# Kernel tuning notes

Measured on AMD Instinct MI355X. Metric: run time of the kernel, lower is better.

The kernel has to match this reference:

```python
import jax, jax.numpy as jnp
import numpy as np

B = 131072
SD, AD, HID = 24, 8, 32
NH = SD + AD            # n_heads = 32
UNITS = HID * NH        # 1024


def _xavier(k, shape):
    fan_in, fan_out = shape[-2], shape[-1]
    lim = float(np.sqrt(6.0 / (fan_in + fan_out)))
    return jax.random.uniform(k, shape, jnp.float32, -lim, lim)


def setup_inputs() -> dict:
    key = jax.random.key(0)
    ks = jax.random.split(key, 8)
    return dict(
        state=jax.random.normal(ks[0], (B, SD), jnp.float32),
        action=jax.random.normal(ks[1], (B, AD), jnp.float32),
        # ripple layer 1: per-head Linear(NH -> HID), gate logits init 0 (init_prob=0.5)
        W1=_xavier(ks[2], (NH, NH, HID)), b1=jnp.zeros((NH, HID), jnp.float32), g1=jnp.zeros((NH,), jnp.float32),
        # ripple layer 2: per-head Linear(UNITS -> HID)
        W2=_xavier(ks[3], (NH, UNITS, HID)), b2=jnp.zeros((NH, HID), jnp.float32), g2=jnp.zeros((NH,), jnp.float32),
        # q_network
        Wq1=_xavier(ks[4], (UNITS, 256)), bq1=jnp.zeros((256,), jnp.float32),
        ln1_g=jnp.ones((256,), jnp.float32), ln1_b=jnp.zeros((256,), jnp.float32),
        Wq2=_xavier(ks[5], (256, 128)), bq2=jnp.zeros((128,), jnp.float32),
        ln2_g=jnp.ones((128,), jnp.float32), ln2_b=jnp.zeros((128,), jnp.float32),
        Wq3=_xavier(ks[6], (128, 1)), bq3=jnp.zeros((1,), jnp.float32),
    )


def _ripple(x, W, b, g):
    # x: [B, D]; W: [H, D, K]; per-head linear + tanh, scaled by per-head sigmoid gate
    h = jnp.tanh(jnp.einsum('bd,hdk->bhk', x, W) + b[None])  # [B, H, K]
    h = h * jax.nn.sigmoid(g)[None, :, None]
    return h.reshape(x.shape[0], -1)  # [B, H*K]


def _ln(x, g, b, eps=1e-5):
    mu = jnp.mean(x, -1, keepdims=True)
    var = jnp.mean((x - mu) ** 2, -1, keepdims=True)
    return (x - mu) * jax.lax.rsqrt(var + eps) * g + b


def reference(state, action, W1, b1, g1, W2, b2, g2,
              Wq1, bq1, ln1_g, ln1_b, Wq2, bq2, ln2_g, ln2_b, Wq3, bq3):
    sa = jnp.concatenate([state, action], axis=1)          # [B, SD+AD]
    x = _ripple(sa, W1, b1, g1)                            # [B, UNITS]
    x = _ripple(x, W2, b2, g2)                             # [B, UNITS]
    h = jax.nn.relu(_ln(x @ Wq1 + bq1, ln1_g, ln1_b))      # [B, 256] (dropout = eval identity)
    h = jax.nn.relu(_ln(h @ Wq2 + bq2, ln2_g, ln2_b))      # [B, 128]
    return h @ Wq3 + bq3                                   # [B, 1]
```

## Files before the change

### kernel.cpp

```cpp
#include <hip/hip_runtime.h>
#include <hip/hip_bf16.h>

typedef _Float16 f16x8 __attribute__((ext_vector_type(8)));
typedef _Float16 f16x4 __attribute__((ext_vector_type(4)));
typedef float f32x4 __attribute__((ext_vector_type(4)));

__device__ __forceinline__ float tanh_fast(float x) {
  float e = __expf(2.0f * x);
  return 1.0f - 2.0f * __builtin_amdgcn_rcpf(e + 1.0f);
}
__device__ __forceinline__ float sigmoid_fast(float x) {
  return __builtin_amdgcn_rcpf(1.0f + __expf(-x));
}

__global__ __launch_bounds__(256) void prep_weights(
    const float* __restrict__ W1, const float* __restrict__ W2,
    const float* __restrict__ Wq1, const float* __restrict__ Wq2,
    _Float16* __restrict__ V1p, _Float16* __restrict__ V2p,
    _Float16* __restrict__ T1p, _Float16* __restrict__ T2p) {
  __shared__ float S[32 * 33];
  int b = blockIdx.x, t = threadIdx.x;
  if (b < 2624) {
    const float* in; _Float16* out; int N, nc0, tile, use_pi;
    if (b < 2048) {
      int h = b >> 6, rem = b & 63, ntl = rem >> 5, kt = rem & 31;
      in = W2 + (size_t)h * 32768 + (size_t)kt * 32 * 32;
      N = 32; nc0 = ntl * 16;
      out = V2p; tile = kt * 64 + (h * 2 + ntl); use_pi = 1;
    } else if (b < 2560) {
      int i = b - 2048, nt = i >> 5, kt = i & 31;
      in = Wq1 + (size_t)kt * 32 * 256; N = 256; nc0 = nt * 16;
      out = T1p; tile = kt * 16 + nt; use_pi = 1;
    } else {
      int i = b - 2560, nt = i >> 3, kt = i & 7;
      in = Wq2 + (size_t)kt * 32 * 128; N = 128; nc0 = nt * 16;
      out = T2p; tile = nt * 8 + kt; use_pi = 0;
    }
    if (t < 128) {
      int r = t >> 2, c4 = (t & 3) * 4;
      const float4 v = *(const float4*)(in + (size_t)r * N + nc0 + c4);
      S[r * 17 + c4 + 0] = v.x; S[r * 17 + c4 + 1] = v.y;
      S[r * 17 + c4 + 2] = v.z; S[r * 17 + c4 + 3] = v.w;
    }
    __syncthreads();
    if (t < 128) {
      int w2 = t >> 6, l = t & 63, q = l >> 4, l15 = l & 15;
      f16x4 o;
#pragma unroll
      for (int jj = 0; jj < 4; ++jj) {
        int kl = use_pi ? (q * 4 + jj + w2 * 16) : (q * 8 + w2 * 4 + jj);
        o[jj] = (_Float16)S[kl * 17 + l15];
      }
      *(f16x4*)(out + (size_t)tile * 512 + l * 8 + w2 * 4) = o;
    }
  } else {
    int h = b - 2624;
    const float* in = W1 + h * 1024;
    int cc = t & 31, rr8 = t >> 5;
#pragma unroll
    for (int p = 0; p < 4; ++p) {
      int r = rr8 + p * 8;
      S[cc * 33 + r] = in[r * 32 + cc];
    }
    __syncthreads();
    if (t < 128) {
      int ntl = t >> 6, l = t & 63, q = l >> 4, l15 = l & 15;
      f16x8 o;
#pragma unroll
      for (int j = 0; j < 8; ++j)
        o[j] = (_Float16)S[(ntl * 16 + l15) * 33 + q * 8 + j];
      *(f16x8*)(V1p + (size_t)(h * 2 + ntl) * 512 + l * 8) = o;
    }
  }
}

__global__ __launch_bounds__(256, 2) void k12_fused(
    const float* __restrict__ state, const float* __restrict__ action,
    const _Float16* __restrict__ v1p, const float* __restrict__ b1,
    const float* __restrict__ g1,
    const _Float16* __restrict__ v2p, const float* __restrict__ b2,
    const float* __restrict__ g2,
    _Float16* __restrict__ x2p, int gro, int NRT) {
  __shared__ __align__(16) _Float16 SA[64 * 40];
  __shared__ __align__(16) _Float16 XF[2 * 8192];
  int g = blockIdx.x;
  int bn = g & 1, bm = g >> 1;
  int t = threadIdx.x, w = t >> 6, l = t & 63, q = l >> 4, l15 = l & 15;
  int wcol = w;
  int m0 = bm * 64;

  {
    int r = t >> 2, qq = t & 3;
    size_t grow = (size_t)(gro + m0 + r);
    const float* src = (qq < 3) ? (state + grow * 24 + qq * 8)
                                : (action + grow * 8);
    float4 v0 = ((const float4*)src)[0];
    float4 v1 = ((const float4*)src)[1];
    float v[8] = {v0.x, v0.y, v0.z, v0.w, v1.x, v1.y, v1.z, v1.w};
    f16x8 h;
#pragma unroll
    for (int j = 0; j < 8; ++j) h[j] = (_Float16)v[j];
    *(f16x8*)&SA[r * 40 + qq * 8] = h;
  }
  __syncthreads();

  f16x8 asa[4];
#pragma unroll
  for (int p = 0; p < 4; ++p)
    asa[p] = *(const f16x8*)&SA[(p * 16 + l15) * 40 + q * 8];

  const int nt0 = bn * 32 + wcol * 8;
  const _Float16* bBase = v2p + (size_t)nt0 * 512 + (size_t)l * 8;
  f32x4 acc[4][8] = {};

  auto Rphase = [&](int kcn) {
    int ktL = kcn * 4 + wcol;
    f16x8 rb0 = *(const f16x8*)(v1p + (size_t)(2 * ktL) * 512 + l * 8);
    f16x8 rb1 = *(const f16x8*)(v1p + (size_t)(2 * ktL + 1) * 512 + l * 8);
    float sg = sigmoid_fast(g1[ktL]);
    f32x4 bs0 = *(const f32x4*)(b1 + ktL * 32 + q * 4);
    f32x4 bs1 = *(const f32x4*)(b1 + ktL * 32 + 16 + q * 4);
    _Float16* bw = XF + ((kcn & 1) * 8192);
#pragma unroll
    for (int p = 0; p < 4; ++p) {
      f32x4 d0 = {}, d1 = {};
      d0 = __builtin_amdgcn_mfma_f32_16x16x32_f16(rb0, asa[p], d0, 0, 0, 0);
      d1 = __builtin_amdgcn_mfma_f32_16x16x32_f16(rb1, asa[p], d1, 0, 0, 0);
      f16x8 o;
#pragma unroll
      for (int r = 0; r < 4; ++r) {
        o[r]     = (_Float16)(tanh_fast(d0[r] + bs0[r]) * sg);
        o[4 + r] = (_Float16)(tanh_fast(d1[r] + bs1[r]) * sg);
      }
      *(f16x8*)(bw + (size_t)(wcol * 4 + p) * 512 + l * 8) = o;
    }
  };

  f16x8 bb0[4], bb1v[4];
#pragma unroll
  for (int n2 = 0; n2 < 4; ++n2)
    bb0[n2] = *(const f16x8*)(bBase + (size_t)n2 * 512);
#pragma unroll
  for (int n2 = 0; n2 < 4; ++n2)
    bb1v[n2] = *(const f16x8*)(bBase + (size_t)(4 + n2) * 512);
  Rphase(0);
  __syncthreads();

#pragma unroll
  for (int kc = 0; kc < 8; ++kc) {
    const _Float16* buf = XF + ((kc & 1) * 8192);
#pragma unroll
    for (int j = 0; j < 4; ++j) {
      if (j == 2 && kc < 7) Rphase(kc + 1);
      int kt = kc * 4 + j;
      f16x8 xa[4];
#pragma unroll
      for (int mi = 0; mi < 4; ++mi)
        xa[mi] = *(const f16x8*)(buf + (size_t)(j * 4 + mi) * 512 + l * 8);
#pragma unroll
      for (int mi = 0; mi < 4; ++mi)
#pragma unroll
        for (int n2 = 0; n2 < 4; ++n2)
          acc[mi][n2] = __builtin_amdgcn_mfma_f32_16x16x32_f16(bb0[n2], xa[mi], acc[mi][n2], 0, 0, 0);
      if (kt < 31) {
#pragma unroll
        for (int n2 = 0; n2 < 4; ++n2)
          bb0[n2] = *(const f16x8*)(bBase + (size_t)((kt + 1) * 64 + n2) * 512);
      }
#pragma unroll
      for (int mi = 0; mi < 4; ++mi)
#pragma unroll
        for (int n2 = 0; n2 < 4; ++n2)
          acc[mi][4 + n2] = __builtin_amdgcn_mfma_f32_16x16x32_f16(bb1v[n2], xa[mi], acc[mi][4 + n2], 0, 0, 0);
      if (kt < 31) {
#pragma unroll
        for (int n2 = 0; n2 < 4; ++n2)
          bb1v[n2] = *(const f16x8*)(bBase + (size_t)((kt + 1) * 64 + 4 + n2) * 512);
      }
    }
    __syncthreads();
  }

#pragma unroll
  for (int mi = 0; mi < 4; ++mi) {
    int rt = bm * 4 + mi;
#pragma unroll
    for (int p2 = 0; p2 < 4; ++p2) {
      int kc2 = (nt0 >> 1) + p2;
      float sg2 = sigmoid_fast(g2[kc2]);
      f32x4 c0 = *(const f32x4*)(b2 + kc2 * 32 + q * 4);
      f32x4 c1 = *(const f32x4*)(b2 + kc2 * 32 + 16 + q * 4);
      f16x8 o;
#pragma unroll
      for (int r = 0; r < 4; ++r) {
        o[r]     = (_Float16)(tanh_fast(acc[mi][2 * p2][r] + c0[r]) * sg2);
        o[4 + r] = (_Float16)(tanh_fast(acc[mi][2 * p2 + 1][r] + c1[r]) * sg2);
      }
      *(f16x8*)(x2p + ((size_t)kc2 * NRT + rt) * 512 + l * 8) = o;
    }
  }
}

__global__ __launch_bounds__(512, 3) void k3_head(
    const _Float16* __restrict__ x2p, const _Float16* __restrict__ t1p,
    const _Float16* __restrict__ t2p,
    const float* __restrict__ bq1, const float* __restrict__ ln1g, const float* __restrict__ ln1b,
    const float* __restrict__ bq2, const float* __restrict__ ln2g, const float* __restrict__ ln2b,
    const float* __restrict__ wq3, const float* __restrict__ bq3,
    float* __restrict__ out, int NRT, int SROWS) {
  __shared__ __align__(16) _Float16 y1h[128 * 264];
  __shared__ float redA[128 * 4], redB[128 * 4];
  __shared__ float meanv[128], rstdv[128];
  int bm = blockIdx.x;
  int t = threadIdx.x, w = t >> 6, l = t & 63, q = l >> 4, l15 = l & 15;
  int wr = w >> 2, wc = w & 3;

  int gt = bm * 8;
  int slice = 0;
  if (gt >= NRT) { slice = 1; gt -= NRT; }
  int rt0 = gt + wr * 4;

  f32x4 acc[4][4] = {};
  const size_t aStep = (size_t)NRT * 512;
  const _Float16* aP = x2p + (size_t)slice * SROWS * 1024 + (size_t)rt0 * 512 + (size_t)l * 8;
  const _Float16* bP = t1p + (size_t)(wc * 4) * 512 + (size_t)l * 8;

  f16x8 a0[4], a1[4], b0[4], b1[4];
#pragma unroll
  for (int mi = 0; mi < 4; ++mi) a0[mi] = *(const f16x8*)(aP + mi * 512);
#pragma unroll
  for (int ni = 0; ni < 4; ++ni) b0[ni] = *(const f16x8*)(bP + ni * 512);
#pragma unroll
  for (int mi = 0; mi < 4; ++mi) a1[mi] = *(const f16x8*)(aP + aStep + mi * 512);
#pragma unroll
  for (int ni = 0; ni < 4; ++ni) b1[ni] = *(const f16x8*)(bP + 8192 + ni * 512);
  aP += 2 * aStep; bP += 16384;

  for (int kt = 0; kt < 32; kt += 2) {
#pragma unroll
    for (int mi = 0; mi < 4; ++mi)
#pragma unroll
      for (int ni = 0; ni < 4; ++ni)
        acc[mi][ni] = __builtin_amdgcn_mfma_f32_16x16x32_f16(a0[mi], b0[ni], acc[mi][ni], 0, 0, 0);
    if (kt < 30) {
#pragma unroll
      for (int mi = 0; mi < 4; ++mi) a0[mi] = *(const f16x8*)(aP + mi * 512);
#pragma unroll
      for (int ni = 0; ni < 4; ++ni) b0[ni] = *(const f16x8*)(bP + ni * 512);
    }
#pragma unroll
    for (int mi = 0; mi < 4; ++mi)
#pragma unroll
      for (int ni = 0; ni < 4; ++ni)
        acc[mi][ni] = __builtin_amdgcn_mfma_f32_16x16x32_f16(a1[mi], b1[ni], acc[mi][ni], 0, 0, 0);
    if (kt < 30) {
#pragma unroll
      for (int mi = 0; mi < 4; ++mi) a1[mi] = *(const f16x8*)(aP + aStep + mi * 512);
#pragma unroll
      for (int ni = 0; ni < 4; ++ni) b1[ni] = *(const f16x8*)(bP + 8192 + ni * 512);
      aP += 2 * aStep; bP += 16384;
    }
  }

#pragma unroll
  for (int ni = 0; ni < 4; ++ni) {
    int col = wc * 64 + ni * 16 + l15;
    float b = bq1[col];
#pragma unroll
    for (int mi = 0; mi < 4; ++mi)
#pragma unroll
      for (int r = 0; r < 4; ++r) acc[mi][ni][r] += b;
  }
#pragma unroll
  for (int mi = 0; mi < 4; ++mi)
#pragma unroll
    for (int r = 0; r < 4; ++r) {
      int row = wr * 64 + mi * 16 + q * 4 + r;
      float s = 0.f, sq = 0.f;
#pragma unroll
      for (int ni = 0; ni < 4; ++ni) { float v = acc[mi][ni][r]; s += v; sq += v * v; }
#pragma unroll
      for (int off = 1; off < 16; off <<= 1) { s += __shfl_xor(s, off); sq += __shfl_xor(sq, off); }
      if (l15 == 0) { redA[row * 4 + wc] = s; redB[row * 4 + wc] = sq; }
    }
  __syncthreads();
  if (t < 128) {
    float s  = redA[t * 4] + redA[t * 4 + 1] + redA[t * 4 + 2] + redA[t * 4 + 3];
    float sq = redB[t * 4] + redB[t * 4 + 1] + redB[t * 4 + 2] + redB[t * 4 + 3];
    float mean = s * (1.0f / 256.0f);
    float var = sq * (1.0f / 256.0f) - mean * mean;
    meanv[t] = mean; rstdv[t] = rsqrtf(var + 1e-5f);
  }
  __syncthreads();
#pragma unroll
  for (int mi = 0; mi < 4; ++mi)
#pragma unroll
    for (int ni = 0; ni < 4; ++ni)
#pragma unroll
      for (int r = 0; r < 4; ++r) {
        int row = wr * 64 + mi * 16 + q * 4 + r;
        int col = wc * 64 + ni * 16 + l15;
        float y = (acc[mi][ni][r] - meanv[row]) * rstdv[row] * ln1g[col] + ln1b[col];
        y = fmaxf(y, 0.f);
        y1h[row * 264 + col] = (_Float16)y;
      }
  __syncthreads();

  f32x4 a2[4][2] = {};
  for (int kt = 0; kt < 8; ++kt) {
    f16x8 af2[4];
#pragma unroll
    for (int mi = 0; mi < 4; ++mi)
      af2[mi] = *(const f16x8*)&y1h[(wr * 64 + mi * 16 + l15) * 264 + kt * 32 + q * 8];
#pragma unroll
    for (int ni = 0; ni < 2; ++ni) {
      f16x8 bf = *(const f16x8*)(t2p + (size_t)(wc * 2 + ni) * 4096 + kt * 512 + l * 8);
#pragma unroll
      for (int mi = 0; mi < 4; ++mi)
        a2[mi][ni] = __builtin_amdgcn_mfma_f32_16x16x32_f16(af2[mi], bf, a2[mi][ni], 0, 0, 0);
    }
  }
#pragma unroll
  for (int ni = 0; ni < 2; ++ni) {
    int col = wc * 32 + ni * 16 + l15;
    float b = bq2[col];
#pragma unroll
    for (int mi = 0; mi < 4; ++mi)
#pragma unroll
      for (int r = 0; r < 4; ++r) a2[mi][ni][r] += b;
  }
  __syncthreads();
#pragma unroll
  for (int mi = 0; mi < 4; ++mi)
#pragma unroll
    for (int r = 0; r < 4; ++r) {
      int row = wr * 64 + mi * 16 + q * 4 + r;
      float s = 0.f, sq = 0.f;
#pragma unroll
      for (int ni = 0; ni < 2; ++ni) { float v = a2[mi][ni][r]; s += v; sq += v * v; }
#pragma unroll
      for (int off = 1; off < 16; off <<= 1) { s += __shfl_xor(s, off); sq += __shfl_xor(sq, off); }
      if (l15 == 0) { redA[row * 4 + wc] = s; redB[row * 4 + wc] = sq; }
    }
  __syncthreads();
  if (t < 128) {
    float s  = redA[t * 4] + redA[t * 4 + 1] + redA[t * 4 + 2] + redA[t * 4 + 3];
    float sq = redB[t * 4] + redB[t * 4 + 1] + redB[t * 4 + 2] + redB[t * 4 + 3];
    float mean = s * (1.0f / 128.0f);
    float var = sq * (1.0f / 128.0f) - mean * mean;
    meanv[t] = mean; rstdv[t] = rsqrtf(var + 1e-5f);
  }
  __syncthreads();
#pragma unroll
  for (int mi = 0; mi < 4; ++mi)
#pragma unroll
    for (int r = 0; r < 4; ++r) {
      int row = wr * 64 + mi * 16 + q * 4 + r;
      float pr = 0.f;
#pragma unroll
      for (int ni = 0; ni < 2; ++ni) {
        int col = wc * 32 + ni * 16 + l15;
        float y = (a2[mi][ni][r] - meanv[row]) * rstdv[row] * ln2g[col] + ln2b[col];
        y = fmaxf(y, 0.f);
        pr += y * wq3[col];
      }
#pragma unroll
      for (int off = 1; off < 16; off <<= 1) pr += __shfl_xor(pr, off);
      if (l15 == 0) redA[row * 4 + wc] = pr;
    }
  __syncthreads();
  if (t < 128)
    out[bm * 128 + t] = redA[t * 4] + redA[t * 4 + 1] + redA[t * 4 + 2] + redA[t * 4 + 3] + bq3[0];
}

extern "C" void kernel_launch(void* const* d_in, const int* in_sizes, int n_in,
                              void* d_out, int out_size, void* d_ws, size_t ws_size,
                              hipStream_t stream) {
  const float* state  = (const float*)d_in[0];
  const float* action = (const float*)d_in[1];
  const float* W1  = (const float*)d_in[2];
  const float* b1  = (const float*)d_in[3];
  const float* g1  = (const float*)d_in[4];
  const float* W2  = (const float*)d_in[5];
  const float* b2  = (const float*)d_in[6];
  const float* g2  = (const float*)d_in[7];
  const float* Wq1 = (const float*)d_in[8];
  const float* bq1 = (const float*)d_in[9];
  const float* ln1g = (const float*)d_in[10];
  const float* ln1b = (const float*)d_in[11];
  const float* Wq2 = (const float*)d_in[12];
  const float* bq2 = (const float*)d_in[13];
  const float* ln2g = (const float*)d_in[14];
  const float* ln2b = (const float*)d_in[15];
  const float* Wq3 = (const float*)d_in[16];
  const float* bq3 = (const float*)d_in[17];
  int B = in_sizes[0] / 24;

  char* ws = (char*)d_ws;
  _Float16* V1p = (_Float16*)(ws);
  _Float16* V2p = (_Float16*)(ws + 65536);
  _Float16* T1p = (_Float16*)(ws + 65536 + 2097152);
  _Float16* T2p = (_Float16*)(ws + 65536 + 2097152 + 524288);
  size_t woff = (65536 + 2097152 + 524288 + 65536 + 4095) & ~(size_t)4095;

  size_t avail = ws_size > woff ? ws_size - woff : 0;
  long rows = (long)(avail / 2048);
  if (rows > 32768) rows = 32768;
  rows &= ~127L;
  if (rows < 128) rows = 128;
  int S = (int)rows;
  _Float16* x2 = (_Float16*)(ws + woff);
  int NRT = S / 16;

  prep_weights<<<2656, 256, 0, stream>>>(W1, W2, Wq1, Wq2, V1p, V2p, T1p, T2p);

  for (int r0 = 0; r0 < B; r0 += S) {
    int Sc = S < (B - r0) ? S : (B - r0);
    int nbm = Sc / 128;
    k12_fused<<<dim3(2 * (Sc / 64)), 256, 0, stream>>>(state, action, V1p, b1, g1,
                                                       V2p, b2, g2, x2, r0, NRT);
    k3_head<<<dim3(nbm), 512, 0, stream>>>(x2, T1p, T2p, bq1, ln1g, ln1b,
                                           bq2, ln2g, ln2b, Wq3, bq3,
                                           (float*)d_out + r0, NRT, S);
  }
}
```

Before: 641.3 us.

## Merge column-half blocks into one 512-thread block to avoid recomputing layer 1

Each k12_fused block now covers all 64 output column tiles for its 64 rows using 8 waves, rather than splitting the columns across two 256-thread blocks. Before, each of those two blocks recomputed the full first ripple layer for the same rows. Layer-1 activations for heads 0-15 and 16-31 are now produced into two halves of an LDS buffer, with the second half computed mid-loop. The A-fragment LDS loads are also double-buffered in registers. The trade-off is a larger LDS footprint per block, fewer blocks in the grid, and heavier register pressure under launch_bounds(512,2).

```diff
diff --git a/kernel.cpp b/kernel.cpp
--- a/kernel.cpp
+++ b/kernel.cpp
@@ -74,7 +74,7 @@
   }
 }
 
-__global__ __launch_bounds__(256, 2) void k12_fused(
+__global__ __launch_bounds__(512, 2) void k12_fused(
     const float* __restrict__ state, const float* __restrict__ action,
     const _Float16* __restrict__ v1p, const float* __restrict__ b1,
     const float* __restrict__ g1,
@@ -82,25 +82,21 @@
     const float* __restrict__ g2,
     _Float16* __restrict__ x2p, int gro, int NRT) {
   __shared__ __align__(16) _Float16 SA[64 * 40];
-  __shared__ __align__(16) _Float16 XF[2 * 8192];
-  int g = blockIdx.x;
-  int bn = g & 1, bm = g >> 1;
+  __shared__ __align__(16) _Float16 XB[2][16 * 4 * 512];
+  int bm = blockIdx.x;
   int t = threadIdx.x, w = t >> 6, l = t & 63, q = l >> 4, l15 = l & 15;
-  int wcol = w;
   int m0 = bm * 64;
 
   {
-    int r = t >> 2, qq = t & 3;
+    int r = t >> 3, qq = t & 7;
     size_t grow = (size_t)(gro + m0 + r);
-    const float* src = (qq < 3) ? (state + grow * 24 + qq * 8)
-                                : (action + grow * 8);
-    float4 v0 = ((const float4*)src)[0];
-    float4 v1 = ((const float4*)src)[1];
-    float v[8] = {v0.x, v0.y, v0.z, v0.w, v1.x, v1.y, v1.z, v1.w};
-    f16x8 h;
-#pragma unroll
-    for (int j = 0; j < 8; ++j) h[j] = (_Float16)v[j];
-    *(f16x8*)&SA[r * 40 + qq * 8] = h;
+    const float* src = (qq < 6) ? (state + grow * 24 + qq * 4)
+                                : (action + grow * 8 + (qq - 6) * 4);
+    float4 v = *(const float4*)src;
+    f16x4 h;
+    h[0] = (_Float16)v.x; h[1] = (_Float16)v.y;
+    h[2] = (_Float16)v.z; h[3] = (_Float16)v.w;
+    *(f16x4*)&SA[r * 40 + qq * 4] = h;
   }
   __syncthreads();
 
@@ -109,18 +105,17 @@
   for (int p = 0; p < 4; ++p)
     asa[p] = *(const f16x8*)&SA[(p * 16 + l15) * 40 + q * 8];
 
-  const int nt0 = bn * 32 + wcol * 8;
+  const int nt0 = w * 8;
   const _Float16* bBase = v2p + (size_t)nt0 * 512 + (size_t)l * 8;
   f32x4 acc[4][8] = {};
 
-  auto Rphase = [&](int kcn) {
-    int ktL = kcn * 4 + wcol;
-    f16x8 rb0 = *(const f16x8*)(v1p + (size_t)(2 * ktL) * 512 + l * 8);
-    f16x8 rb1 = *(const f16x8*)(v1p + (size_t)(2 * ktL + 1) * 512 + l * 8);
-    float sg = sigmoid_fast(g1[ktL]);
-    f32x4 bs0 = *(const f32x4*)(b1 + ktL * 32 + q * 4);
-    f32x4 bs1 = *(const f32x4*)(b1 + ktL * 32 + 16 + q * 4);
-    _Float16* bw = XF + ((kcn & 1) * 8192);
+  auto produce = [&](int h, int buf) {
+    f16x8 rb0 = *(const f16x8*)(v1p + (size_t)(2 * h) * 512 + l * 8);
+    f16x8 rb1 = *(const f16x8*)(v1p + (size_t)(2 * h + 1) * 512 + l * 8);
+    float sg = sigmoid_fast(g1[h]);
+    f32x4 bs0 = *(const f32x4*)(b1 + h * 32 + q * 4);
+    f32x4 bs1 = *(const f32x4*)(b1 + h * 32 + 16 + q * 4);
+    _Float16* bw = &XB[buf][(size_t)((h & 15) * 4) * 512 + l * 8];
 #pragma unroll
     for (int p = 0; p < 4; ++p) {
       f32x4 d0 = {}, d1 = {};
@@ -132,7 +127,7 @@
         o[r]     = (_Float16)(tanh_fast(d0[r] + bs0[r]) * sg);
         o[4 + r] = (_Float16)(tanh_fast(d1[r] + bs1[r]) * sg);
       }
-      *(f16x8*)(bw + (size_t)(wcol * 4 + p) * 512 + l * 8) = o;
+      *(f16x8*)(bw + (size_t)p * 512) = o;
     }
   };
 
@@ -143,42 +138,82 @@
 #pragma unroll
   for (int n2 = 0; n2 < 4; ++n2)
     bb1v[n2] = *(const f16x8*)(bBase + (size_t)(4 + n2) * 512);
-  Rphase(0);
-  __syncthreads();
-
-#pragma unroll
-  for (int kc = 0; kc < 8; ++kc) {
-    const _Float16* buf = XF + ((kc & 1) * 8192);
-#pragma unroll
-    for (int j = 0; j < 4; ++j) {
-      if (j == 2 && kc < 7) Rphase(kc + 1);
-      int kt = kc * 4 + j;
-      f16x8 xa[4];
+  produce(w * 2, 0);
+  produce(w * 2 + 1, 0);
+  __syncthreads();
+
+  f16x8 xab[2][4];
+#pragma unroll
+  for (int mi = 0; mi < 4; ++mi)
+    xab[0][mi] = *(const f16x8*)&XB[0][(size_t)mi * 512 + l * 8];
+
+#pragma unroll
+  for (int ktl = 0; ktl < 16; ++ktl) {
+    int kt = ktl;
+    if (ktl == 6)  produce(16 + w * 2, 1);
+    if (ktl == 10) produce(16 + w * 2 + 1, 1);
+    if (ktl < 15) {
 #pragma unroll
       for (int mi = 0; mi < 4; ++mi)
-        xa[mi] = *(const f16x8*)(buf + (size_t)(j * 4 + mi) * 512 + l * 8);
+        xab[(ktl + 1) & 1][mi] =
+            *(const f16x8*)&XB[0][(size_t)((ktl + 1) * 4 + mi) * 512 + l * 8];
+    }
+#pragma unroll
+    for (int mi = 0; mi < 4; ++mi)
+#pragma unroll
+      for (int n2 = 0; n2 < 4; ++n2)
+        acc[mi][n2] = __builtin_amdgcn_mfma_f32_16x16x32_f16(
+            bb0[n2], xab[ktl & 1][mi], acc[mi][n2], 0, 0, 0);
+#pragma unroll
+    for (int n2 = 0; n2 < 4; ++n2)
+      bb0[n2] = *(const f16x8*)(bBase + (size_t)((kt + 1) * 64 + n2) * 512);
+#pragma unroll
+    for (int mi = 0; mi < 4; ++mi)
+#pragma unroll
+      for (int n2 = 0; n2 < 4; ++n2)
+        acc[mi][4 + n2] = __builtin_amdgcn_mfma_f32_16x16x32_f16(
+            bb1v[n2], xab[ktl & 1][mi], acc[mi][4 + n2], 0, 0, 0);
+#pragma unroll
+    for (int n2 = 0; n2 < 4; ++n2)
+      bb1v[n2] = *(const f16x8*)(bBase + (size_t)((kt + 1) * 64 + 4 + n2) * 512);
+  }
+  __syncthreads();
+
+#pragma unroll
+  for (int mi = 0; mi < 4; ++mi)
+    xab[0][mi] = *(const f16x8*)&XB[1][(size_t)mi * 512 + l * 8];
+
+#pragma unroll
+  for (int ktl = 0; ktl < 16; ++ktl) {
+    int kt = 16 + ktl;
+    if (ktl < 15) {
 #pragma unroll
       for (int mi = 0; mi < 4; ++mi)
-#pragma unroll
-        for (int n2 = 0; n2 < 4; ++n2)
-          acc[mi][n2] = __builtin_amdgcn_mfma_f32_16x16x32_f16(bb0[n2], xa[mi], acc[mi][n2], 0, 0, 0);
-      if (kt < 31) {
-#pragma unroll
-        for (int n2 = 0; n2 < 4; ++n2)
-          bb0[n2] = *(const f16x8*)(bBase + (size_t)((kt + 1) * 64 + n2) * 512);
-      }
-#pragma unroll
-      for (int mi = 0; mi < 4; ++mi)
-#pragma unroll
-        for (int n2 = 0; n2 < 4; ++n2)
-          acc[mi][4 + n2] = __builtin_amdgcn_mfma_f32_16x16x32_f16(bb1v[n2], xa[mi], acc[mi][4 + n2], 0, 0, 0);
-      if (kt < 31) {
-#pragma unroll
-        for (int n2 = 0; n2 < 4; ++n2)
-          bb1v[n2] = *(const f16x8*)(bBase + (size_t)((kt + 1) * 64 + 4 + n2) * 512);
-      }
-    }
-    __syncthreads();
+        xab[(ktl + 1) & 1][mi] =
+            *(const f16x8*)&XB[1][(size_t)((ktl + 1) * 4 + mi) * 512 + l * 8];
+    }
+#pragma unroll
+    for (int mi = 0; mi < 4; ++mi)
+#pragma unroll
+      for (int n2 = 0; n2 < 4; ++n2)
+        acc[mi][n2] = __builtin_amdgcn_mfma_f32_16x16x32_f16(
+            bb0[n2], xab[ktl & 1][mi], acc[mi][n2], 0, 0, 0);
+    if (kt < 31) {
+#pragma unroll
+      for (int n2 = 0; n2 < 4; ++n2)
+        bb0[n2] = *(const f16x8*)(bBase + (size_t)((kt + 1) * 64 + n2) * 512);
+    }
+#pragma unroll
+    for (int mi = 0; mi < 4; ++mi)
+#pragma unroll
+      for (int n2 = 0; n2 < 4; ++n2)
+        acc[mi][4 + n2] = __builtin_amdgcn_mfma_f32_16x16x32_f16(
+            bb1v[n2], xab[ktl & 1][mi], acc[mi][4 + n2], 0, 0, 0);
+    if (kt < 31) {
+#pragma unroll
+      for (int n2 = 0; n2 < 4; ++n2)
+        bb1v[n2] = *(const f16x8*)(bBase + (size_t)((kt + 1) * 64 + 4 + n2) * 512);
+    }
   }
 
 #pragma unroll
@@ -417,8 +452,8 @@
   for (int r0 = 0; r0 < B; r0 += S) {
     int Sc = S < (B - r0) ? S : (B - r0);
     int nbm = Sc / 128;
-    k12_fused<<<dim3(2 * (Sc / 64)), 256, 0, stream>>>(state, action, V1p, b1, g1,
-                                                       V2p, b2, g2, x2, r0, NRT);
+    k12_fused<<<dim3(Sc / 64), 512, 0, stream>>>(state, action, V1p, b1, g1,
+                                                 V2p, b2, g2, x2, r0, NRT);
     k3_head<<<dim3(nbm), 512, 0, stream>>>(x2, T1p, T2p, bq1, ln1g, ln1b,
                                            bq2, ln2g, ln2b, Wq3, bq3,
                                            (float*)d_out + r0, NRT, S);
```

Result: faster. 565.7 us (-11.8%).
